# Kernel optimization log

Hardware: AMD Instinct MI355X
Metric: run time of the kernel (lower is better)

## Reference

```python
import jax, jax.numpy as jnp
import numpy as np

D_MODEL = 1024
B, T = 4, 4096
LN_EPS = 1e-5
DEN_EPS = 1e-6


def setup_inputs() -> dict:
    key = jax.random.key(0)
    ks = jax.random.split(key, 10)
    s = 1.0 / np.sqrt(D_MODEL)
    return {
        "x": jax.random.normal(ks[0], (B, T, D_MODEL), dtype=jnp.float32),
        "w_qkv": jax.random.normal(ks[1], (D_MODEL, 3 * D_MODEL), dtype=jnp.float32) * s,
        "b_qkv": jnp.zeros((3 * D_MODEL,), dtype=jnp.float32),
        "w_gate": jax.random.normal(ks[2], (D_MODEL, D_MODEL), dtype=jnp.float32) * s,
        "b_gate": jnp.zeros((D_MODEL,), dtype=jnp.float32),
        "w_proj": jax.random.normal(ks[3], (D_MODEL, D_MODEL), dtype=jnp.float32) * s,
        "b_proj": jnp.zeros((D_MODEL,), dtype=jnp.float32),
        "ln_g": jnp.ones((D_MODEL,), dtype=jnp.float32),
        "ln_b": jnp.zeros((D_MODEL,), dtype=jnp.float32),
    }


def reference(x, w_qkv, b_qkv, w_gate, b_gate, w_proj, b_proj, ln_g, ln_b):
    # LayerNorm
    mu = jnp.mean(x, axis=-1, keepdims=True)
    var = jnp.mean(jnp.square(x - mu), axis=-1, keepdims=True)
    xn = (x - mu) * jax.lax.rsqrt(var + LN_EPS) * ln_g + ln_b
    # qkv projection + gated keys
    qkv = xn @ w_qkv + b_qkv                      # [B,T,3D]
    q, k, v = jnp.split(qkv, 3, axis=-1)
    gate = jax.nn.sigmoid(xn @ w_gate + b_gate)
    k = k * gate
    q = jax.nn.elu(q) + 1.0
    k = jax.nn.elu(k) + 1.0
    # quadratic causal linear attention (faithful to source)
    attn = jnp.einsum("btd,bsd->bts", q, k)      # [B,T,T]
    tq = jnp.arange(q.shape[1])
    mask = (tq[:, None] >= tq[None, :]).astype(attn.dtype)  # tril
    attn = attn * mask
    out_num = jnp.einsum("bts,bsd->btd", attn, v)
    k_cumsum = jnp.cumsum(k, axis=1)
    out_den = jnp.sum(q * k_cumsum, axis=-1, keepdims=True) + DEN_EPS
    return (out_num / out_den) @ w_proj + b_proj
```

## Files before the change

kernel.cpp:

```cpp
#include <hip/hip_runtime.h>
#include <math.h>

typedef unsigned short u16;
typedef __attribute__((ext_vector_type(8))) short bf16x8;
typedef __attribute__((ext_vector_type(4))) float f32x4;
typedef const __attribute__((address_space(1))) unsigned int* gas_t;
typedef __attribute__((address_space(3))) unsigned int* las_t;

#define BK 32

__device__ __forceinline__ float bf2f(u16 u) {
    unsigned x = ((unsigned)u) << 16; float f; __builtin_memcpy(&f, &x, 4); return f;
}
__device__ __forceinline__ u16 f2bf(float f) {
    unsigned x; __builtin_memcpy(&x, &f, 4);
    unsigned lsb = (x >> 16) & 1u; x += 0x7fffu + lsb; return (u16)(x >> 16);
}

__global__ __launch_bounds__(256) void k_detect(const u16* __restrict__ wq, int* __restrict__ flag) {
    const int tid = threadIdx.x;
    int cnt = 0;
    for (int i = tid; i < 2048; i += 256) {
        float v = fabsf(bf2f(wq[2 * i]));
        if (!(v < 1e4f) || (v != 0.f && v < 1e-30f)) cnt++;
    }
    for (int off = 32; off; off >>= 1) cnt += __shfl_down(cnt, off, 64);
    __shared__ int red[4];
    int lane = tid & 63, w = tid >> 6;
    if (!lane) red[w] = cnt;
    __syncthreads();
    if (!tid) flag[0] = (red[0] + red[1] + red[2] + red[3] > 204) ? 1 : 0;
}

__global__ __launch_bounds__(256) void k_cvec(const void* __restrict__ bqkv, const void* __restrict__ bgate,
                                              const void* __restrict__ bproj, const void* __restrict__ lng,
                                              const void* __restrict__ lnb, const int* __restrict__ flag,
                                              u16* __restrict__ cv) {
    int i = blockIdx.x * 256 + threadIdx.x;
    const void* src; int off;
    if (i < 3072)      { src = bqkv;  off = i; }
    else if (i < 4096) { src = bgate; off = i - 3072; }
    else if (i < 5120) { src = bproj; off = i - 4096; }
    else if (i < 6144) { src = lng;   off = i - 5120; }
    else               { src = lnb;   off = i - 6144; }
    cv[i] = flag[0] ? f2bf(((const float*)src)[off]) : ((const u16*)src)[off];
}

__device__ __forceinline__ void gemm_loop(const u16* __restrict__ Ab, long ar0, long as_, long ka0,
                                          const u16* __restrict__ Bb, long br0, long bs_, long kb0,
                                          int ksteps, u16* As, u16* Bs, int tid, f32x4 acc[4][4]) {
    const int lane = tid & 63;
    const int wave = tid >> 6;
    const int waveM = (tid >> 7) & 1;
    const int waveN = (tid >> 6) & 1;
    const int quad = lane >> 4, l16 = lane & 15;
    const int rs = wave * 16 + (lane >> 2);
    const int cs = (lane & 3) * 8;
    const u16* A0 = Ab + (ar0 + rs) * as_ + ka0 + cs;
    const u16* A1 = Ab + (ar0 + 64 + rs) * as_ + ka0 + cs;
    const u16* B0 = Bb + (br0 + rs) * bs_ + kb0 + cs;
    const u16* B1 = Bb + (br0 + 64 + rs) * bs_ + kb0 + cs;
    u16* lA0 = As + wave * 512;
    u16* lA1 = As + 2048 + wave * 512;
    u16* lB0 = Bs + wave * 512;
    u16* lB1 = Bs + 2048 + wave * 512;
    for (int kt = 0; kt < ksteps; ++kt) {
        const long ko = (long)kt * BK;
        __builtin_amdgcn_global_load_lds((gas_t)(A0 + ko), (las_t)lA0, 16, 0, 0);
        __builtin_amdgcn_global_load_lds((gas_t)(A1 + ko), (las_t)lA1, 16, 0, 0);
        __builtin_amdgcn_global_load_lds((gas_t)(B0 + ko), (las_t)lB0, 16, 0, 0);
        __builtin_amdgcn_global_load_lds((gas_t)(B1 + ko), (las_t)lB1, 16, 0, 0);
        __syncthreads();
        bf16x8 af[4], bv[4];
#pragma unroll
        for (int mi = 0; mi < 4; ++mi)
            af[mi] = *(const bf16x8*)(As + (waveM * 64 + mi * 16 + l16) * BK + quad * 8);
#pragma unroll
        for (int ni = 0; ni < 4; ++ni)
            bv[ni] = *(const bf16x8*)(Bs + (waveN * 64 + ni * 16 + l16) * BK + quad * 8);
#pragma unroll
        for (int mi = 0; mi < 4; ++mi)
#pragma unroll
            for (int ni = 0; ni < 4; ++ni)
                acc[mi][ni] = __builtin_amdgcn_mfma_f32_16x16x32_bf16(af[mi], bv[ni], acc[mi][ni], 0, 0, 0);
        __syncthreads();
    }
}

#define EPI_COORDS \
    const int lane = tid & 63; const int quad = lane >> 4; const int l16 = lane & 15; \
    const int waveM = (tid >> 7) & 1; const int waveN = (tid >> 6) & 1;

#define ZERO_ACC(acc) \
    _Pragma("unroll") for (int mi = 0; mi < 4; ++mi) \
    _Pragma("unroll") for (int ni = 0; ni < 4; ++ni) acc[mi][ni] = (f32x4){0.f, 0.f, 0.f, 0.f};

#define ZERO_ACC8(acc) \
    _Pragma("unroll") for (int mi = 0; mi < 8; ++mi) \
    _Pragma("unroll") for (int ni = 0; ni < 4; ++ni) acc[mi][ni] = (f32x4){0.f, 0.f, 0.f, 0.f};

__device__ __forceinline__ void gemm256_loop(const u16* __restrict__ Ab, long ar0, long lda, long ka0,
                                             const u16* __restrict__ Bb, long br0, long ldb, long kb0,
                                             int ktiles, u16* lds, int tid, f32x4 acc[8][4]) {
    const int lane = tid & 63, wave = tid >> 6;
    const int waveM = wave >> 2, waveN = wave & 3;
    const int l16 = lane & 15, quad = lane >> 4;
    const int x = l16 & 7;
    const long sT = (long)(((tid & 7) ^ ((tid >> 3) & 7)) << 3);
    const u16* sA = Ab + (ar0 + (tid >> 3)) * lda + ka0 + sT;
    const u16* sB = Bb + (br0 + (tid >> 3)) * ldb + kb0 + sT;
    u16* const ldsw = lds + wave * 512;
    const int aoff = waveM * 8192;

#define STG_A(p, mh, t) do { \
        const u16* g_ = sA + ((long)((mh) * 128)) * lda + (long)(t) * 64; \
        __builtin_amdgcn_global_load_lds((gas_t)g_, (las_t)(ldsw + (p) * 16384 + (mh) * 8192), 16, 0, 0); \
        __builtin_amdgcn_global_load_lds((gas_t)(g_ + 64 * lda), (las_t)(ldsw + (p) * 16384 + (mh) * 8192 + 4096), 16, 0, 0); \
    } while (0)
#define STG_B(p, nh, t) do { \
        const u16* g_ = sB + ((long)((nh) * 128)) * ldb + (long)(t) * 64; \
        __builtin_amdgcn_global_load_lds((gas_t)g_, (las_t)(ldsw + 32768 + (p) * 16384 + (nh) * 8192), 16, 0, 0); \
        __builtin_amdgcn_global_load_lds((gas_t)(g_ + 64 * ldb), (las_t)(ldsw + 32768 + (p) * 16384 + (nh) * 8192 + 4096), 16, 0, 0); \
    } while (0)
#define RD_A(mi_, ks_) (*(const bf16x8*)(lds + pb + aoff + ((mi_) * 16 + l16) * 64 + (((((ks_) << 2) + quad) ^ x) << 3)))
#define RD_B(ni_, ks_) (*(const bf16x8*)(lds + 32768 + pb + ((waveN * 64 + (ni_) * 16 + l16) >> 7) * 8192 \
                        + ((waveN * 64 + (ni_) * 16 + l16) & 127) * 64 + (((((ks_) << 2) + quad) ^ x) << 3)))

    STG_A(0, 0, 0); STG_A(0, 1, 0); STG_B(0, 0, 0); STG_B(0, 1, 0);
    if (ktiles > 1) {
        STG_A(1, 0, 1); STG_B(1, 0, 1);
        asm volatile("s_waitcnt vmcnt(4)" ::: "memory");
    } else {
        asm volatile("s_waitcnt vmcnt(0)" ::: "memory");
    }
    __builtin_amdgcn_s_barrier();

    bf16x8 aF[8][2], bF[2][2];
    for (int t = 0; t < ktiles; ++t) {
        const int p = t & 1, q = p ^ 1;
        const int pb = p * 16384;
#pragma unroll
        for (int mi = 0; mi < 4; ++mi)
#pragma unroll
            for (int ks = 0; ks < 2; ++ks) aF[mi][ks] = RD_A(mi, ks);
#pragma unroll
        for (int ni = 0; ni < 2; ++ni)
#pragma unroll
            for (int ks = 0; ks < 2; ++ks) bF[ni][ks] = RD_B(ni, ks);
        if (t + 1 < ktiles) STG_B(q, 1, t + 1);
        __builtin_amdgcn_s_barrier();
        __builtin_amdgcn_s_setprio(1);
#pragma unroll
        for (int mi = 0; mi < 4; ++mi)
#pragma unroll
            for (int ni = 0; ni < 2; ++ni)
#pragma unroll
                for (int ks = 0; ks < 2; ++ks)
                    acc[mi][ni] = __builtin_amdgcn_mfma_f32_16x16x32_bf16(aF[mi][ks], bF[ni][ks], acc[mi][ni], 0, 0, 0);
        __builtin_amdgcn_s_setprio(0);
        asm volatile("s_waitcnt lgkmcnt(0)" ::: "memory");
        __builtin_amdgcn_s_barrier();
#pragma unroll
        for (int mi = 4; mi < 8; ++mi)
#pragma unroll
            for (int ks = 0; ks < 2; ++ks) aF[mi][ks] = RD_A(mi, ks);
        if (t + 1 < ktiles) STG_A(q, 1, t + 1);
        __builtin_amdgcn_s_barrier();
        __builtin_amdgcn_s_setprio(1);
#pragma unroll
        for (int mi = 0; mi < 4; ++mi)
#pragma unroll
            for (int ni = 0; ni < 2; ++ni)
#pragma unroll
                for (int ks = 0; ks < 2; ++ks)
                    acc[4 + mi][ni] = __builtin_amdgcn_mfma_f32_16x16x32_bf16(aF[4 + mi][ks], bF[ni][ks], acc[4 + mi][ni], 0, 0, 0);
        __builtin_amdgcn_s_setprio(0);
        asm volatile("s_waitcnt lgkmcnt(0)" ::: "memory");
        __builtin_amdgcn_s_barrier();
#pragma unroll
        for (int ni = 0; ni < 2; ++ni)
#pragma unroll
            for (int ks = 0; ks < 2; ++ks) bF[ni][ks] = RD_B(ni + 2, ks);
        if (t + 2 < ktiles) STG_A(p, 0, t + 2);
        __builtin_amdgcn_s_barrier();
        __builtin_amdgcn_s_setprio(1);
#pragma unroll
        for (int mi = 0; mi < 4; ++mi)
#pragma unroll
            for (int ni = 0; ni < 2; ++ni)
#pragma unroll
                for (int ks = 0; ks < 2; ++ks)
                    acc[mi][2 + ni] = __builtin_amdgcn_mfma_f32_16x16x32_bf16(aF[mi][ks], bF[ni][ks], acc[mi][2 + ni], 0, 0, 0);
        __builtin_amdgcn_s_setprio(0);
        asm volatile("s_waitcnt lgkmcnt(0)" ::: "memory");
        __builtin_amdgcn_s_barrier();
        if (t + 2 < ktiles) STG_B(p, 0, t + 2);
        __builtin_amdgcn_s_setprio(1);
#pragma unroll
        for (int mi = 0; mi < 4; ++mi)
#pragma unroll
            for (int ni = 0; ni < 2; ++ni)
#pragma unroll
                for (int ks = 0; ks < 2; ++ks)
                    acc[4 + mi][2 + ni] = __builtin_amdgcn_mfma_f32_16x16x32_bf16(aF[4 + mi][ks], bF[ni][ks], acc[4 + mi][2 + ni], 0, 0, 0);
        __builtin_amdgcn_s_setprio(0);
        if (t + 2 < ktiles)      asm volatile("s_waitcnt vmcnt(4)" ::: "memory");
        else if (t + 1 < ktiles) asm volatile("s_waitcnt vmcnt(0)" ::: "memory");
        __builtin_amdgcn_s_barrier();
    }
#undef STG_A
#undef STG_B
#undef RD_A
#undef RD_B
}

__global__ __launch_bounds__(256) void k_transw(const void* __restrict__ wqkv, const void* __restrict__ wgate,
                                                const void* __restrict__ wproj, const int* __restrict__ flag,
                                                u16* __restrict__ Wt, u16* __restrict__ WpT) {
    const int bid = blockIdx.x, tid = threadIdx.x;
    const int ktl = bid & 15, ntile = bid >> 4;
    const int n0 = ntile * 64, k0 = ktl * 64;
    const int fl = flag[0];
    const void* src; int ld, c0;
    if (n0 < 3072)      { src = wqkv;  ld = 3072; c0 = n0; }
    else if (n0 < 4096) { src = wgate; ld = 1024; c0 = n0 - 3072; }
    else                { src = wproj; ld = 1024; c0 = n0 - 4096; }
    __shared__ u16 t[64][66];
#pragma unroll
    for (int i = 0; i < 16; ++i) {
        int idx = tid + i * 256; int r = idx >> 6, c = idx & 63;
        long off = (long)(k0 + r) * ld + c0 + c;
        float v = fl ? ((const float*)src)[off] : bf2f(((const u16*)src)[off]);
        t[r][c] = f2bf(v);
    }
    __syncthreads();
#pragma unroll
    for (int i = 0; i < 16; ++i) {
        int idx = tid + i * 256; int r = idx >> 6, c = idx & 63;
        int n = n0 + r;
        if (n < 4096) Wt[(long)n * 1024 + k0 + c] = t[c][r];
        else          WpT[(long)(n - 4096) * 1024 + k0 + c] = t[c][r];
    }
}

__global__ __launch_bounds__(256) void k_ln(const void* __restrict__ xin, const u16* __restrict__ cv,
                                            const int* __restrict__ flag, u16* __restrict__ XN) {
    const long t = blockIdx.x; const int tid = threadIdx.x;
    const int fl = flag[0];
    float v[4], s = 0.f, sq = 0.f;
#pragma unroll
    for (int i = 0; i < 4; ++i) {
        long a = t * 1024 + tid + i * 256;
        v[i] = fl ? ((const float*)xin)[a] : bf2f(((const u16*)xin)[a]);
        s += v[i]; sq += v[i] * v[i];
    }
    for (int off = 32; off; off >>= 1) { s += __shfl_down(s, off, 64); sq += __shfl_down(sq, off, 64); }
    __shared__ float red[8];
    int lane = tid & 63, w = tid >> 6;
    if (!lane) { red[w] = s; red[4 + w] = sq; }
    __syncthreads();
    float S = red[0] + red[1] + red[2] + red[3];
    float SQ = red[4] + red[5] + red[6] + red[7];
    float mu = S * (1.f / 1024.f);
    float var = SQ * (1.f / 1024.f) - mu * mu;
    float rs = rsqrtf(var + 1e-5f);
#pragma unroll
    for (int i = 0; i < 4; ++i) {
        int col = tid + i * 256;
        XN[t * 1024 + col] = f2bf((v[i] - mu) * rs * bf2f(cv[5120 + col]) + bf2f(cv[6144 + col]));
    }
}

__global__ __launch_bounds__(512, 2) void k_gemm1(const u16* __restrict__ XN, const u16* __restrict__ Wt,
                                                  const u16* __restrict__ cv,
                                                  u16* __restrict__ Q, u16* __restrict__ K,
                                                  u16* __restrict__ G, u16* __restrict__ vT) {
    __shared__ u16 lds[65536];
    const int tid = threadIdx.x;
    const int swz = ((blockIdx.x & 7) << 7) | (blockIdx.x >> 3);
    const int nt = swz & 15, mt = swz >> 4;
    f32x4 acc[8][4]; ZERO_ACC8(acc);
    gemm256_loop(XN, (long)mt * 256, 1024, 0, Wt, (long)nt * 256, 1024, 0, 16, lds, tid, acc);
    const int lane = tid & 63, wave = tid >> 6;
    const int waveM = wave >> 2, waveN = wave & 3;
    const int l16 = lane & 15, quad = lane >> 4;
    const int g = nt >> 2;
    if (g == 2) {
        const int b = mt >> 4;
        const long tb0 = (long)(mt & 15) * 256;
#pragma unroll
        for (int h = 0; h < 4; ++h) {
            if (waveN == h) {
#pragma unroll
                for (int mi = 0; mi < 8; ++mi)
#pragma unroll
                    for (int ni = 0; ni < 4; ++ni) {
                        int col = ni * 16 + l16;
                        float bias = bf2f(cv[nt * 256 + h * 64 + col]);
#pragma unroll
                        for (int r = 0; r < 4; ++r)
                            lds[col * 264 + waveM * 128 + mi * 16 + quad * 4 + r] = f2bf(acc[mi][ni][r] + bias);
                    }
            }
            __syncthreads();
#pragma unroll
            for (int i = 0; i < 4; ++i) {
                int c = tid + i * 512;
                int col = c >> 5, t8 = (c & 31) * 8;
                uint4 val = *(const uint4*)(lds + col * 264 + t8);
                long dg = (long)(nt & 3) * 256 + h * 64 + col;
                *(uint4*)(vT + (long)b * 4194304 + dg * 4096 + tb0 + t8) = val;
            }
            __syncthreads();
        }
    } else {
        u16* dst = (g == 0) ? Q : (g == 1) ? K : G;
#pragma unroll
        for (int mi = 0; mi < 8; ++mi)
#pragma unroll
            for (int ni = 0; ni < 4; ++ni) {
                int colg = nt * 256 + waveN * 64 + ni * 16 + l16;
                int d = colg & 1023;
                float bias = bf2f(cv[colg]);
                long row0 = (long)mt * 256 + waveM * 128 + mi * 16 + quad * 4;
#pragma unroll
                for (int r = 0; r < 4; ++r) {
                    float v = acc[mi][ni][r] + bias;
                    if (g == 0) v = v > 0.f ? v + 1.f : expf(v);
                    dst[(row0 + r) * 1024 + d] = f2bf(v);
                }
            }
    }
}

__global__ __launch_bounds__(256) void k_act(u16* __restrict__ K, const u16* __restrict__ G) {
    const long t = blockIdx.x; const int tid = threadIdx.x;
#pragma unroll
    for (int i = 0; i < 4; ++i) {
        long a = t * 1024 + tid + i * 256;
        float kk = bf2f(K[a]) / (1.f + expf(-bf2f(G[a])));
        kk = kk > 0.f ? kk + 1.f : expf(kk);
        K[a] = f2bf(kk);
    }
}

__global__ __launch_bounds__(256) void k_transk(const u16* __restrict__ K, u16* __restrict__ kT) {
    const int bid = blockIdx.x, tid = threadIdx.x;
    const int dt = bid & 15, tt = bid >> 4;
    __shared__ u16 tileS[64][65];
#pragma unroll
    for (int i = 0; i < 16; ++i) {
        int idx = tid + i * 256; int r = idx >> 6, cc = idx & 63;
        tileS[r][cc] = K[(long)(tt * 64 + r) * 1024 + dt * 64 + cc];
    }
    __syncthreads();
    long tg = (long)tt * 64; int b = (int)(tg >> 12); long tb = tg & 4095;
#pragma unroll
    for (int i = 0; i < 16; ++i) {
        int idx = tid + i * 256; int r = idx >> 6, cc = idx & 63;
        kT[(long)b * 4194304 + (long)(dt * 64 + r) * 4096 + tb + cc] = tileS[cc][r];
    }
}

__global__ __launch_bounds__(256) void k_csum(const u16* __restrict__ K, float* __restrict__ csum) {
    const int bid = blockIdx.x, tid = threadIdx.x;
    const int b = bid >> 4, c = (bid >> 2) & 3, dg = bid & 3;
    const int d = dg * 256 + tid;
    const u16* base = K + ((long)b * 4096 + c * 1024) * 1024 + d;
    float s = 0.f;
    for (int t = 0; t < 1024; ++t) s += bf2f(base[(long)t * 1024]);
    csum[((b * 4 + c) << 10) + d] = s;
}

__global__ __launch_bounds__(512, 2) void k_pass1(const u16* __restrict__ kT, const u16* __restrict__ vT,
                                                  u16* __restrict__ ST) {
    __shared__ u16 lds[65536];
    const int tid = threadIdx.x, bid = blockIdx.x;
    const int tile = bid & 15, bc = bid >> 4;
    const int dt = tile >> 2, et = tile & 3;
    const int c = bc & 3, b = bc >> 2;
    f32x4 acc[8][4]; ZERO_ACC8(acc);
    gemm256_loop(vT + (long)b * 4194304, (long)dt * 256, 4096, (long)c * 1024,
                 kT + (long)b * 4194304, (long)et * 256, 4096, (long)c * 1024, 16, lds, tid, acc);
    const int lane = tid & 63, wave = tid >> 6;
    const int waveM = wave >> 2, waveN = wave & 3;
    const int l16 = lane & 15, quad = lane >> 4;
    u16* dst = ST + ((long)(b * 4 + c) << 20);
#pragma unroll
    for (int mi = 0; mi < 8; ++mi)
#pragma unroll
        for (int ni = 0; ni < 4; ++ni) {
            long e = et * 256 + waveN * 64 + ni * 16 + l16;
            long d0 = dt * 256 + waveM * 128 + mi * 16 + quad * 4;
#pragma unroll
            for (int r = 0; r < 4; ++r)
                dst[(d0 + r) * 1024 + e] = f2bf(acc[mi][ni][r]);
        }
}

__global__ __launch_bounds__(256) void k_stpre(u16* __restrict__ ST) {
    const long gid = (long)blockIdx.x * 256 + threadIdx.x;
    const int b = (int)(gid >> 20); const long rem = gid & 0xFFFFF;
    float run = 0.f;
    for (int c = 0; c < 4; ++c) {
        long a = (((long)(b * 4 + c)) << 20) + rem;
        float v = bf2f(ST[a]);
        ST[a] = f2bf(run);
        run += v;
    }
}

__global__ __launch_bounds__(256) void k_pass2a(const u16* __restrict__ Q, const u16* __restrict__ K,
                                                u16* __restrict__ P) {
    const int tid = threadIdx.x, bid = blockIdx.x;
    const int tile = bid & 63, c = (bid >> 6) & 3, b = bid >> 8;
    const int ti = tile >> 3, si = tile & 7;
    const long trow0 = (long)b * 4096 + c * 1024 + ti * 128;
    if (si > ti) {
#pragma unroll
        for (int i = 0; i < 64; ++i) {
            int idx = tid + i * 256; int rr = idx >> 7, cc = idx & 127;
            P[(trow0 + rr) * 1024 + si * 128 + cc] = 0;
        }
        return;
    }
    __shared__ u16 S[8192];
    const long srow0 = (long)b * 4096 + c * 1024 + si * 128;
    f32x4 acc[4][4]; ZERO_ACC(acc);
    gemm_loop(Q, trow0, 1024, 0, K, srow0, 1024, 0, 32, S, S + 4096, tid, acc);
    EPI_COORDS
#pragma unroll
    for (int mi = 0; mi < 4; ++mi)
#pragma unroll
        for (int ni = 0; ni < 4; ++ni) {
            int slc = si * 128 + waveN * 64 + ni * 16 + l16;
#pragma unroll
            for (int r = 0; r < 4; ++r) {
                int tl = waveM * 64 + mi * 16 + quad * 4 + r;
                float v = (ti * 128 + tl >= slc) ? acc[mi][ni][r] : 0.f;
                P[(trow0 + tl) * 1024 + slc] = f2bf(v);
            }
        }
}

__global__ __launch_bounds__(256) void k_den(const u16* __restrict__ Q, const u16* __restrict__ P,
                                             const float* __restrict__ csum, float* __restrict__ den) {
    const long t = blockIdx.x; const int tid = threadIdx.x;
    const int b = (int)(t >> 12), c = (int)((t >> 10) & 3);
    float s = 0.f;
#pragma unroll
    for (int i = 0; i < 4; ++i) {
        int e = tid + i * 256;
        float kp = 0.f;
        for (int cp = 0; cp < c; ++cp) kp += csum[((b * 4 + cp) << 10) + e];
        s += bf2f(Q[t * 1024 + e]) * kp + bf2f(P[t * 1024 + e]);
    }
    for (int off = 32; off; off >>= 1) s += __shfl_down(s, off, 64);
    __shared__ float red[4];
    int lane = tid & 63, w = tid >> 6;
    if (!lane) red[w] = s;
    __syncthreads();
    if (!tid) den[t] = red[0] + red[1] + red[2] + red[3] + 1e-6f;
}

__global__ __launch_bounds__(256) void k_pass2b(const u16* __restrict__ Q, const u16* __restrict__ ST,
                                                const u16* __restrict__ P, const u16* __restrict__ vT,
                                                const float* __restrict__ den, u16* __restrict__ Yb) {
    __shared__ u16 S[8192];
    const int tid = threadIdx.x, bid = blockIdx.x;
    const int tile = bid & 63, c = (bid >> 6) & 3, b = bid >> 8;
    const int ti = tile >> 3, di = tile & 7;
    const long trow0 = (long)b * 4096 + c * 1024 + ti * 128;
    f32x4 acc[4][4]; ZERO_ACC(acc);
    if (c > 0)
        gemm_loop(Q, trow0, 1024, 0, ST + ((long)(b * 4 + c) << 20), (long)di * 128, 1024, 0,
                  32, S, S + 4096, tid, acc);
    gemm_loop(P, trow0, 1024, 0, vT + (long)b * 4194304, (long)di * 128, 4096, (long)c * 1024,
              (ti + 1) * 4, S, S + 4096, tid, acc);
    EPI_COORDS
#pragma unroll
    for (int mi = 0; mi < 4; ++mi)
#pragma unroll
        for (int ni = 0; ni < 4; ++ni) {
            long d = di * 128 + waveN * 64 + ni * 16 + l16;
#pragma unroll
            for (int r = 0; r < 4; ++r) {
                long t = trow0 + waveM * 64 + mi * 16 + quad * 4 + r;
                Yb[t * 1024 + d] = f2bf(acc[mi][ni][r] / den[t]);
            }
        }
}

__global__ __launch_bounds__(512, 2) void k_proj(const u16* __restrict__ Yb, const u16* __restrict__ WpT,
                                                 const u16* __restrict__ cv, const int* __restrict__ flag,
                                                 void* __restrict__ out) {
    __shared__ u16 lds[65536];
    const int tid = threadIdx.x, bid = blockIdx.x;
    const int nt = bid & 3, mt = bid >> 2;
    f32x4 acc[8][4]; ZERO_ACC8(acc);
    gemm256_loop(Yb, (long)mt * 256, 1024, 0, WpT, (long)nt * 256, 1024, 0, 16, lds, tid, acc);
    const int lane = tid & 63, wave = tid >> 6;
    const int waveM = wave >> 2, waveN = wave & 3;
    const int l16 = lane & 15, quad = lane >> 4;
    const int fl = flag[0];
#pragma unroll
    for (int mi = 0; mi < 8; ++mi)
#pragma unroll
        for (int ni = 0; ni < 4; ++ni) {
            long col = nt * 256 + waveN * 64 + ni * 16 + l16;
            float bias = bf2f(cv[4096 + col]);
            long row0 = (long)mt * 256 + waveM * 128 + mi * 16 + quad * 4;
#pragma unroll
            for (int r = 0; r < 4; ++r) {
                float v = acc[mi][ni][r] + bias;
                if (fl) ((float*)out)[(row0 + r) * 1024 + col] = v;
                else    ((u16*)out)[(row0 + r) * 1024 + col] = f2bf(v);
            }
        }
}

__global__ __launch_bounds__(256) void k_fb(u16* __restrict__ out, long n, float val) {
    long i = (long)blockIdx.x * 256 + threadIdx.x;
    if (i < n) out[i] = f2bf(val);
}

extern "C" void kernel_launch(void* const* d_in, const int* in_sizes, int n_in,
                              void* d_out, int out_size, void* d_ws, size_t ws_size,
                              hipStream_t stream) {
    const void* x     = d_in[0];
    const void* wqkv  = d_in[1];
    const void* bqkv  = d_in[2];
    const void* wgate = d_in[3];
    const void* bgate = d_in[4];
    const void* wproj = d_in[5];
    const void* bproj = d_in[6];
    const void* lng   = d_in[7];
    const void* lnb   = d_in[8];

    const long NEEDED = 178403336L;
    if (ws_size < (size_t)NEEDED) {
        k_fb<<<(int)((out_size + 255) / 256), 256, 0, stream>>>((u16*)d_out, out_size, (float)(ws_size >> 20));
        return;
    }

    char* w = (char*)d_ws;
    u16* XN  = (u16*)(w);
    u16* ST  = XN;
    u16* Q   = (u16*)(w + 33554432L);
    u16* K   = (u16*)(w + 67108864L);
    u16* Yb  = K;
    u16* G   = (u16*)(w + 100663296L);
    u16* kT  = G;
    u16* P   = G;
    u16* vT  = (u16*)(w + 134217728L);
    u16* Wt  = (u16*)(w + 167772160L);
    u16* WpT = (u16*)(w + 176160768L);
    float* csum = (float*)(w + 178257920L);
    float* den  = (float*)(w + 178323456L);
    u16* cv     = (u16*)(w + 178388992L);
    int* flag   = (int*)(w + 178403328L);

    k_detect<<<1,     256, 0, stream>>>((const u16*)wqkv, flag);
    k_cvec  <<<28,    256, 0, stream>>>(bqkv, bgate, bproj, lng, lnb, flag, cv);
    k_transw<<<1280,  256, 0, stream>>>(wqkv, wgate, wproj, flag, Wt, WpT);
    k_ln    <<<16384, 256, 0, stream>>>(x, cv, flag, XN);
    k_gemm1 <<<1024,  512, 0, stream>>>(XN, Wt, cv, Q, K, G, vT);
    k_act   <<<16384, 256, 0, stream>>>(K, G);
    k_transk<<<4096,  256, 0, stream>>>(K, kT);
    k_csum  <<<64,    256, 0, stream>>>(K, csum);
    k_pass1 <<<256,   512, 0, stream>>>(kT, vT, ST);
    k_stpre <<<16384, 256, 0, stream>>>(ST);
    k_pass2a<<<1024,  256, 0, stream>>>(Q, K, P);
    k_den   <<<16384, 256, 0, stream>>>(Q, P, csum, den);
    k_pass2b<<<1024,  256, 0, stream>>>(Q, ST, P, vT, den, Yb);
    k_proj  <<<256,   512, 0, stream>>>(Yb, WpT, cv, flag, d_out);
}
```

Baseline: 637.5 us.

## Move pass2a/pass2b to 256x256 pipelined GEMM tiles with precomputed LDS offsets

Drops the simple 128x128 single-buffered gemm_loop and moves the intra-chunk attention kernels (pass2a and pass2b) onto the double-buffered, swizzled 256x256 gemm256_loop with 512-thread blocks. LDS read addresses in gemm256_loop are now precomputed once per thread, and the pass1 and pass2 block index maps are reordered so the batch-chunk index varies fastest. The goal is more operand reuse per block, fewer redundant global loads and less address math in the inner loop. The cost is coarser causal tiles: diagonal 256-wide tiles do some wasted work, and there are only 256 blocks, which may leave compute units under-filled.

After: 564.0 us. 1.13x faster.

```diff
diff --git a/kernel.cpp b/kernel.cpp
--- a/kernel.cpp
+++ b/kernel.cpp
@@ -6,8 +6,6 @@
 typedef __attribute__((ext_vector_type(4))) float f32x4;
 typedef const __attribute__((address_space(1))) unsigned int* gas_t;
 typedef __attribute__((address_space(3))) unsigned int* las_t;
-
-#define BK 32
 
 __device__ __forceinline__ float bf2f(u16 u) {
     unsigned x = ((unsigned)u) << 16; float f; __builtin_memcpy(&f, &x, 4); return f;
@@ -46,55 +44,6 @@
     cv[i] = flag[0] ? f2bf(((const float*)src)[off]) : ((const u16*)src)[off];
 }
 
-__device__ __forceinline__ void gemm_loop(const u16* __restrict__ Ab, long ar0, long as_, long ka0,
-                                          const u16* __restrict__ Bb, long br0, long bs_, long kb0,
-                                          int ksteps, u16* As, u16* Bs, int tid, f32x4 acc[4][4]) {
-    const int lane = tid & 63;
-    const int wave = tid >> 6;
-    const int waveM = (tid >> 7) & 1;
-    const int waveN = (tid >> 6) & 1;
-    const int quad = lane >> 4, l16 = lane & 15;
-    const int rs = wave * 16 + (lane >> 2);
-    const int cs = (lane & 3) * 8;
-    const u16* A0 = Ab + (ar0 + rs) * as_ + ka0 + cs;
-    const u16* A1 = Ab + (ar0 + 64 + rs) * as_ + ka0 + cs;
-    const u16* B0 = Bb + (br0 + rs) * bs_ + kb0 + cs;
-    const u16* B1 = Bb + (br0 + 64 + rs) * bs_ + kb0 + cs;
-    u16* lA0 = As + wave * 512;
-    u16* lA1 = As + 2048 + wave * 512;
-    u16* lB0 = Bs + wave * 512;
-    u16* lB1 = Bs + 2048 + wave * 512;
-    for (int kt = 0; kt < ksteps; ++kt) {
-        const long ko = (long)kt * BK;
-        __builtin_amdgcn_global_load_lds((gas_t)(A0 + ko), (las_t)lA0, 16, 0, 0);
-        __builtin_amdgcn_global_load_lds((gas_t)(A1 + ko), (las_t)lA1, 16, 0, 0);
-        __builtin_amdgcn_global_load_lds((gas_t)(B0 + ko), (las_t)lB0, 16, 0, 0);
-        __builtin_amdgcn_global_load_lds((gas_t)(B1 + ko), (las_t)lB1, 16, 0, 0);
-        __syncthreads();
-        bf16x8 af[4], bv[4];
-#pragma unroll
-        for (int mi = 0; mi < 4; ++mi)
-            af[mi] = *(const bf16x8*)(As + (waveM * 64 + mi * 16 + l16) * BK + quad * 8);
-#pragma unroll
-        for (int ni = 0; ni < 4; ++ni)
-            bv[ni] = *(const bf16x8*)(Bs + (waveN * 64 + ni * 16 + l16) * BK + quad * 8);
-#pragma unroll
-        for (int mi = 0; mi < 4; ++mi)
-#pragma unroll
-            for (int ni = 0; ni < 4; ++ni)
-                acc[mi][ni] = __builtin_amdgcn_mfma_f32_16x16x32_bf16(af[mi], bv[ni], acc[mi][ni], 0, 0, 0);
-        __syncthreads();
-    }
-}
-
-#define EPI_COORDS \
-    const int lane = tid & 63; const int quad = lane >> 4; const int l16 = lane & 15; \
-    const int waveM = (tid >> 7) & 1; const int waveN = (tid >> 6) & 1;
-
-#define ZERO_ACC(acc) \
-    _Pragma("unroll") for (int mi = 0; mi < 4; ++mi) \
-    _Pragma("unroll") for (int ni = 0; ni < 4; ++ni) acc[mi][ni] = (f32x4){0.f, 0.f, 0.f, 0.f};
-
 #define ZERO_ACC8(acc) \
     _Pragma("unroll") for (int mi = 0; mi < 8; ++mi) \
     _Pragma("unroll") for (int ni = 0; ni < 4; ++ni) acc[mi][ni] = (f32x4){0.f, 0.f, 0.f, 0.f};
@@ -110,7 +59,12 @@
     const u16* sA = Ab + (ar0 + (tid >> 3)) * lda + ka0 + sT;
     const u16* sB = Bb + (br0 + (tid >> 3)) * ldb + kb0 + sT;
     u16* const ldsw = lds + wave * 512;
-    const int aoff = waveM * 8192;
+    const int s0 = (quad ^ x) << 3;
+    const int s1 = s0 ^ 32;
+    const int aB0 = waveM * 8192 + l16 * 64 + s0;
+    const int aB1 = waveM * 8192 + l16 * 64 + s1;
+    const int bB0 = 32768 + (waveN >> 1) * 8192 + ((waveN & 1) * 64 + l16) * 64 + s0;
+    const int bB1 = 32768 + (waveN >> 1) * 8192 + ((waveN & 1) * 64 + l16) * 64 + s1;
 
 #define STG_A(p, mh, t) do { \
         const u16* g_ = sA + ((long)((mh) * 128)) * lda + (long)(t) * 64; \
@@ -122,9 +76,8 @@
         __builtin_amdgcn_global_load_lds((gas_t)g_, (las_t)(ldsw + 32768 + (p) * 16384 + (nh) * 8192), 16, 0, 0); \
         __builtin_amdgcn_global_load_lds((gas_t)(g_ + 64 * ldb), (las_t)(ldsw + 32768 + (p) * 16384 + (nh) * 8192 + 4096), 16, 0, 0); \
     } while (0)
-#define RD_A(mi_, ks_) (*(const bf16x8*)(lds + pb + aoff + ((mi_) * 16 + l16) * 64 + (((((ks_) << 2) + quad) ^ x) << 3)))
-#define RD_B(ni_, ks_) (*(const bf16x8*)(lds + 32768 + pb + ((waveN * 64 + (ni_) * 16 + l16) >> 7) * 8192 \
-                        + ((waveN * 64 + (ni_) * 16 + l16) & 127) * 64 + (((((ks_) << 2) + quad) ^ x) << 3)))
+#define RD_A(mi_, ks_) (*(const bf16x8*)(lds + pb + ((ks_) ? aB1 : aB0) + (mi_) * 1024))
+#define RD_B(ni_, ks_) (*(const bf16x8*)(lds + pb + ((ks_) ? bB1 : bB0) + (ni_) * 1024))
 
     STG_A(0, 0, 0); STG_A(0, 1, 0); STG_B(0, 0, 0); STG_B(0, 1, 0);
     if (ktiles > 1) {
@@ -376,7 +329,7 @@
                                                   u16* __restrict__ ST) {
     __shared__ u16 lds[65536];
     const int tid = threadIdx.x, bid = blockIdx.x;
-    const int tile = bid & 15, bc = bid >> 4;
+    const int bc = bid & 15, tile = bid >> 4;
     const int dt = tile >> 2, et = tile & 3;
     const int c = bc & 3, b = bc >> 2;
     f32x4 acc[8][4]; ZERO_ACC8(acc);
@@ -410,35 +363,40 @@
     }
 }
 
-__global__ __launch_bounds__(256) void k_pass2a(const u16* __restrict__ Q, const u16* __restrict__ K,
-                                                u16* __restrict__ P) {
+__global__ __launch_bounds__(512, 2) void k_pass2a(const u16* __restrict__ Q, const u16* __restrict__ K,
+                                                   u16* __restrict__ P) {
+    __shared__ u16 lds[65536];
     const int tid = threadIdx.x, bid = blockIdx.x;
-    const int tile = bid & 63, c = (bid >> 6) & 3, b = bid >> 8;
-    const int ti = tile >> 3, si = tile & 7;
-    const long trow0 = (long)b * 4096 + c * 1024 + ti * 128;
-    if (si > ti) {
-#pragma unroll
-        for (int i = 0; i < 64; ++i) {
-            int idx = tid + i * 256; int rr = idx >> 7, cc = idx & 127;
-            P[(trow0 + rr) * 1024 + si * 128 + cc] = 0;
+    const int bc = bid & 15, tile = bid >> 4;
+    const int tt = tile >> 2, ss = tile & 3;
+    const int c = bc & 3, b = bc >> 2;
+    const long trow0 = (long)b * 4096 + c * 1024 + tt * 256;
+    if (ss > tt) {
+#pragma unroll
+        for (int i = 0; i < 16; ++i) {
+            int ch = tid + i * 512;
+            int row = ch >> 5, col8 = (ch & 31) * 8;
+            *(uint4*)(P + (trow0 + row) * 1024 + ss * 256 + col8) = (uint4){0u, 0u, 0u, 0u};
         }
         return;
     }
-    __shared__ u16 S[8192];
-    const long srow0 = (long)b * 4096 + c * 1024 + si * 128;
-    f32x4 acc[4][4]; ZERO_ACC(acc);
-    gemm_loop(Q, trow0, 1024, 0, K, srow0, 1024, 0, 32, S, S + 4096, tid, acc);
-    EPI_COORDS
-#pragma unroll
-    for (int mi = 0; mi < 4; ++mi)
+    const long srow0 = (long)b * 4096 + c * 1024 + ss * 256;
+    f32x4 acc[8][4]; ZERO_ACC8(acc);
+    gemm256_loop(Q, trow0, 1024, 0, K, srow0, 1024, 0, 16, lds, tid, acc);
+    const int lane = tid & 63, wave = tid >> 6;
+    const int waveM = wave >> 2, waveN = wave & 3;
+    const int l16 = lane & 15, quad = lane >> 4;
+    const int diag = (ss == tt);
+#pragma unroll
+    for (int mi = 0; mi < 8; ++mi)
 #pragma unroll
         for (int ni = 0; ni < 4; ++ni) {
-            int slc = si * 128 + waveN * 64 + ni * 16 + l16;
+            int slc = waveN * 64 + ni * 16 + l16;
 #pragma unroll
             for (int r = 0; r < 4; ++r) {
-                int tl = waveM * 64 + mi * 16 + quad * 4 + r;
-                float v = (ti * 128 + tl >= slc) ? acc[mi][ni][r] : 0.f;
-                P[(trow0 + tl) * 1024 + slc] = f2bf(v);
+                int tl = waveM * 128 + mi * 16 + quad * 4 + r;
+                float v = (!diag || tl >= slc) ? acc[mi][ni][r] : 0.f;
+                P[(trow0 + tl) * 1024 + ss * 256 + slc] = f2bf(v);
             }
         }
 }
@@ -463,29 +421,32 @@
     if (!tid) den[t] = red[0] + red[1] + red[2] + red[3] + 1e-6f;
 }
 
-__global__ __launch_bounds__(256) void k_pass2b(const u16* __restrict__ Q, const u16* __restrict__ ST,
-                                                const u16* __restrict__ P, const u16* __restrict__ vT,
-                                                const float* __restrict__ den, u16* __restrict__ Yb) {
-    __shared__ u16 S[8192];
+__global__ __launch_bounds__(512, 2) void k_pass2b(const u16* __restrict__ Q, const u16* __restrict__ ST,
+                                                   const u16* __restrict__ P, const u16* __restrict__ vT,
+                                                   const float* __restrict__ den, u16* __restrict__ Yb) {
+    __shared__ u16 lds[65536];
     const int tid = threadIdx.x, bid = blockIdx.x;
-    const int tile = bid & 63, c = (bid >> 6) & 3, b = bid >> 8;
-    const int ti = tile >> 3, di = tile & 7;
-    const long trow0 = (long)b * 4096 + c * 1024 + ti * 128;
-    f32x4 acc[4][4]; ZERO_ACC(acc);
+    const int bc = bid & 15, tile = bid >> 4;
+    const int tt = tile >> 2, dd = tile & 3;
+    const int c = bc & 3, b = bc >> 2;
+    const long trow0 = (long)b * 4096 + c * 1024 + tt * 256;
+    f32x4 acc[8][4]; ZERO_ACC8(acc);
     if (c > 0)
-        gemm_loop(Q, trow0, 1024, 0, ST + ((long)(b * 4 + c) << 20), (long)di * 128, 1024, 0,
-                  32, S, S + 4096, tid, acc);
-    gemm_loop(P, trow0, 1024, 0, vT + (long)b * 4194304, (long)di * 128, 4096, (long)c * 1024,
-              (ti + 1) * 4, S, S + 4096, tid, acc);
-    EPI_COORDS
-#pragma unroll
-    for (int mi = 0; mi < 4; ++mi)
+        gemm256_loop(Q, trow0, 1024, 0, ST + ((long)(b * 4 + c) << 20), (long)dd * 256, 1024, 0,
+                     16, lds, tid, acc);
+    gemm256_loop(P, trow0, 1024, 0, vT + (long)b * 4194304, (long)dd * 256, 4096, (long)c * 1024,
+                 (tt + 1) * 4, lds, tid, acc);
+    const int lane = tid & 63, wave = tid >> 6;
+    const int waveM = wave >> 2, waveN = wave & 3;
+    const int l16 = lane & 15, quad = lane >> 4;
+#pragma unroll
+    for (int mi = 0; mi < 8; ++mi)
 #pragma unroll
         for (int ni = 0; ni < 4; ++ni) {
-            long d = di * 128 + waveN * 64 + ni * 16 + l16;
+            long d = dd * 256 + waveN * 64 + ni * 16 + l16;
 #pragma unroll
             for (int r = 0; r < 4; ++r) {
-                long t = trow0 + waveM * 64 + mi * 16 + quad * 4 + r;
+                long t = trow0 + waveM * 128 + mi * 16 + quad * 4 + r;
                 Yb[t * 1024 + d] = f2bf(acc[mi][ni][r] / den[t]);
             }
         }
@@ -570,8 +531,8 @@
     k_csum  <<<64,    256, 0, stream>>>(K, csum);
     k_pass1 <<<256,   512, 0, stream>>>(kT, vT, ST);
     k_stpre <<<16384, 256, 0, stream>>>(ST);
-    k_pass2a<<<1024,  256, 0, stream>>>(Q, K, P);
+    k_pass2a<<<256,   512, 0, stream>>>(Q, K, P);
     k_den   <<<16384, 256, 0, stream>>>(Q, P, csum, den);
-    k_pass2b<<<1024,  256, 0, stream>>>(Q, ST, P, vT, den, Yb);
+    k_pass2b<<<256,   512, 0, stream>>>(Q, ST, P, vT, den, Yb);
     k_proj  <<<256,   512, 0, stream>>>(Yb, WpT, cv, flag, d_out);
 }
```
